# Optimization experiments

Measured on AMD Instinct MI355X. Metric: run time of the kernel, lower is better.

Reference implementation:

```python
import jax, jax.numpy as jnp
import numpy as np

D_MODEL = 2048
NUM_HEADS = 16
HEAD_DIM = D_MODEL // NUM_HEADS
D_FF = 4 * D_MODEL
B, L = 2, 2048
LN_EPS = 1e-6


def layer_norm(x, scale, bias):
    x32 = x.astype(jnp.float32)
    mu = jnp.mean(x32, axis=-1, keepdims=True)
    var = jnp.mean(jnp.square(x32 - mu), axis=-1, keepdims=True)
    return (x32 - mu) * jax.lax.rsqrt(var + LN_EPS) * scale + bias


def setup_inputs() -> dict:
    key = jax.random.key(0)
    ks = jax.random.split(key, 10)
    s = 1.0 / np.sqrt(D_MODEL)
    x = jax.random.normal(ks[0], (B, L, D_MODEL), dtype=jnp.float32)
    mask = jnp.tril(jnp.ones((L, L), dtype=bool))[None, None, :, :]  # causal [1,1,L,L]
    wq = jax.random.normal(ks[1], (D_MODEL, D_MODEL), jnp.float32) * s
    wk = jax.random.normal(ks[2], (D_MODEL, D_MODEL), jnp.float32) * s
    wv = jax.random.normal(ks[3], (D_MODEL, D_MODEL), jnp.float32) * s
    wo = jax.random.normal(ks[4], (D_MODEL, D_MODEL), jnp.float32) * s
    w1 = jax.random.normal(ks[5], (D_MODEL, D_FF), jnp.float32) * s
    b1 = jnp.zeros((D_FF,), jnp.float32)
    w2 = jax.random.normal(ks[6], (D_FF, D_MODEL), jnp.float32) * (1.0 / np.sqrt(D_FF))
    b2 = jnp.zeros((D_MODEL,), jnp.float32)
    ln1_scale = jnp.ones((D_MODEL,), jnp.float32)
    ln1_bias = jnp.zeros((D_MODEL,), jnp.float32)
    ln2_scale = jnp.ones((D_MODEL,), jnp.float32)
    ln2_bias = jnp.zeros((D_MODEL,), jnp.float32)
    return {"x": x, "mask": mask, "ln1_scale": ln1_scale, "ln1_bias": ln1_bias,
            "wq": wq, "wk": wk, "wv": wv, "wo": wo,
            "ln2_scale": ln2_scale, "ln2_bias": ln2_bias,
            "w1": w1, "b1": b1, "w2": w2, "b2": b2}


def reference(x, mask, ln1_scale, ln1_bias, wq, wk, wv, wo,
              ln2_scale, ln2_bias, w1, b1, w2, b2):
    residual = x
    h = layer_norm(x, ln1_scale, ln1_bias)
    b, l, _ = h.shape
    q = (h @ wq).reshape(b, l, NUM_HEADS, HEAD_DIM)
    k = (h @ wk).reshape(b, l, NUM_HEADS, HEAD_DIM)
    v = (h @ wv).reshape(b, l, NUM_HEADS, HEAD_DIM)
    scores = jnp.einsum('bqhd,bkhd->bhqk', q, k) / jnp.sqrt(jnp.float32(HEAD_DIM))
    scores = jnp.where(mask, scores, -100000.0)
    attn = jax.nn.softmax(scores, axis=-1)
    attn_out = jnp.einsum('bhqk,bkhd->bqhd', attn, v).reshape(b, l, D_MODEL)
    x = residual + attn_out @ wo
    mlp = jax.nn.gelu(layer_norm(x, ln2_scale, ln2_bias) @ w1 + b1)
    return x + mlp @ w2 + b2
```

## Files before the change

### kernel.cpp

```cpp
#include <hip/hip_runtime.h>
#include <hip/hip_bf16.h>

typedef unsigned short u16;
typedef __bf16 bf16x8 __attribute__((ext_vector_type(8)));
typedef float f32x4 __attribute__((ext_vector_type(4)));

#define D_MODEL 2048
#define D_FF    8192
#define NH      16
#define HD      128
#define BATCH   2
#define SEQ     2048
#define ROWS    (BATCH*SEQ)

__device__ __forceinline__ u16 f2bf(float f) {
  union { __hip_bfloat16 h; u16 u; } cv;
  cv.h = __float2bfloat16(f);
  return cv.u;
}

__device__ __forceinline__ void gload16(const u16* g, u16* l) {
  __builtin_amdgcn_global_load_lds((const __attribute__((address_space(1))) void*)g,
                                   (__attribute__((address_space(3))) void*)l,
                                   16, 0, 0);
}

__device__ __forceinline__ float gelu_f(float x) {
  const float k0 = 0.7978845608028654f, k1 = 0.044715f;
  return 0.5f * x * (1.0f + tanhf(k0 * (x + k1 * x * x * x)));
}

__global__ __launch_bounds__(256) void ln_bf16_kernel(
    const float* __restrict__ x, const float* __restrict__ sc,
    const float* __restrict__ bs, u16* __restrict__ out)
{
  __shared__ float red[8];
  const int row = blockIdx.x, t = threadIdx.x;
  const int w = t >> 6, l = t & 63;
  const float* xr = x + (size_t)row * D_MODEL;
  float4 a = ((const float4*)xr)[t*2];
  float4 b = ((const float4*)xr)[t*2+1];
  float s  = a.x+a.y+a.z+a.w + b.x+b.y+b.z+b.w;
  float s2 = a.x*a.x+a.y*a.y+a.z*a.z+a.w*a.w + b.x*b.x+b.y*b.y+b.z*b.z+b.w*b.w;
  for (int off = 32; off; off >>= 1) { s += __shfl_down(s, off); s2 += __shfl_down(s2, off); }
  if (l == 0) { red[w] = s; red[4+w] = s2; }
  __syncthreads();
  s  = red[0]+red[1]+red[2]+red[3];
  s2 = red[4]+red[5]+red[6]+red[7];
  const float mu  = s * (1.0f / D_MODEL);
  const float var = s2 * (1.0f / D_MODEL) - mu * mu;
  const float inv = rsqrtf(var + 1e-6f);
  float4 g0 = ((const float4*)sc)[t*2], g1 = ((const float4*)sc)[t*2+1];
  float4 q0 = ((const float4*)bs)[t*2], q1 = ((const float4*)bs)[t*2+1];
  union { u16 u[8]; uint4 v; } o;
  o.u[0] = f2bf((a.x-mu)*inv*g0.x + q0.x);
  o.u[1] = f2bf((a.y-mu)*inv*g0.y + q0.y);
  o.u[2] = f2bf((a.z-mu)*inv*g0.z + q0.z);
  o.u[3] = f2bf((a.w-mu)*inv*g0.w + q0.w);
  o.u[4] = f2bf((b.x-mu)*inv*g1.x + q1.x);
  o.u[5] = f2bf((b.y-mu)*inv*g1.y + q1.y);
  o.u[6] = f2bf((b.z-mu)*inv*g1.z + q1.z);
  o.u[7] = f2bf((b.w-mu)*inv*g1.w + q1.w);
  *(uint4*)(&out[(size_t)row * D_MODEL + t*8]) = o.v;
}

__global__ __launch_bounds__(256) void transpose_w(
    const float* __restrict__ in, u16* __restrict__ out, int R, int C)
{
  __shared__ float tile[64][65];
  const int t = threadIdx.x;
  const int c0 = blockIdx.x*64, r0 = blockIdx.y*64;
  const int cq = (t & 15) * 4, rb = t >> 4;
#pragma unroll
  for (int i = 0; i < 4; ++i) {
    const float4 v = *(const float4*)&in[(size_t)(r0 + rb + i*16)*C + c0 + cq];
    tile[rb + i*16][cq+0] = v.x; tile[rb + i*16][cq+1] = v.y;
    tile[rb + i*16][cq+2] = v.z; tile[rb + i*16][cq+3] = v.w;
  }
  __syncthreads();
#pragma unroll
  for (int i = 0; i < 4; ++i) {
    const int oc = rb + i*16;
    ushort4 o;
    o.x = f2bf(tile[cq+0][oc]); o.y = f2bf(tile[cq+1][oc]);
    o.z = f2bf(tile[cq+2][oc]); o.w = f2bf(tile[cq+3][oc]);
    *(ushort4*)&out[(size_t)(c0 + oc)*R + r0 + cq] = o;
  }
}

__global__ __launch_bounds__(256) void transpose_w4(
    const float* __restrict__ s0, const float* __restrict__ s1,
    const float* __restrict__ s2, const float* __restrict__ s3,
    u16* __restrict__ d0, u16* __restrict__ d1,
    u16* __restrict__ d2, u16* __restrict__ d3)
{
  __shared__ float tile[64][65];
  const int z = blockIdx.z;
  const float* in = (z == 0) ? s0 : (z == 1) ? s1 : (z == 2) ? s2 : s3;
  u16* out       = (z == 0) ? d0 : (z == 1) ? d1 : (z == 2) ? d2 : d3;
  const int t = threadIdx.x;
  const int c0 = blockIdx.x*64, r0 = blockIdx.y*64;
  const int cq = (t & 15) * 4, rb = t >> 4;
#pragma unroll
  for (int i = 0; i < 4; ++i) {
    const float4 v = *(const float4*)&in[(size_t)(r0 + rb + i*16)*D_MODEL + c0 + cq];
    tile[rb + i*16][cq+0] = v.x; tile[rb + i*16][cq+1] = v.y;
    tile[rb + i*16][cq+2] = v.z; tile[rb + i*16][cq+3] = v.w;
  }
  __syncthreads();
#pragma unroll
  for (int i = 0; i < 4; ++i) {
    const int oc = rb + i*16;
    ushort4 o;
    o.x = f2bf(tile[cq+0][oc]); o.y = f2bf(tile[cq+1][oc]);
    o.z = f2bf(tile[cq+2][oc]); o.w = f2bf(tile[cq+3][oc]);
    *(ushort4*)&out[(size_t)(c0 + oc)*D_MODEL + r0 + cq] = o;
  }
}

__global__ __launch_bounds__(256) void transpose_v(
    const u16* __restrict__ qkv, u16* __restrict__ vt)
{
  __shared__ u16 tile[32][34];
  const int t = threadIdx.x;
  const int b = blockIdx.z;
  const int c0 = blockIdx.x*32, r0 = blockIdx.y*32;
  const int col = t & 31, rb = t >> 5;
  const u16* inb = qkv + (size_t)b*SEQ*3*D_MODEL + 2*D_MODEL;
#pragma unroll
  for (int i = 0; i < 4; ++i)
    tile[rb+i*8][col] = inb[(size_t)(r0+rb+i*8)*(3*D_MODEL) + c0+col];
  __syncthreads();
  u16* ob = vt + (size_t)b*SEQ*D_MODEL;
#pragma unroll
  for (int i = 0; i < 4; ++i)
    ob[(size_t)(c0+rb+i*8)*SEQ + r0+col] = tile[col][rb+i*8];
}

template<int EPI, int BNP>
__global__ __launch_bounds__(512, 1) void gemm8p(
    const u16* __restrict__ A, const u16* __restrict__ BT,
    void* __restrict__ Cout, const float* __restrict__ bias,
    const float* __restrict__ res, int N, int K, int gridN)
{
  constexpr int GB    = BNP / 128;
  constexpr int NI    = BNP / 64;
  constexpr int BHALF = BNP * 32;
  constexpr int BUFU  = 16384 + BNP * 64;
  __shared__ __align__(16) u16 lds[2 * BUFU];
  const int t = threadIdx.x;
  const int nwg = gridDim.x;
  const int wg = (int)blockIdx.x;
  const int wgid = (wg & 7) * (nwg >> 3) + (wg >> 3);
  const int bx = wgid % gridN, by = wgid / gridN;
  const int m0 = by * 256, n0 = bx * BNP;
  const int w = t >> 6, l = t & 63;
  const int wm = w >> 2, wn = w & 3;
  const int l15 = l & 15, lq = l >> 4;

  const int srow = t >> 2;
  const int c0s  = (t & 3) ^ ((srow >> 1) & 3);
  const u16* aS0 = A  + (size_t)(m0 + srow) * K + c0s * 8;
  const u16* aS1 = A  + (size_t)(m0 + 128 + srow) * K + c0s * 8;
  const u16* bS0 = BT + (size_t)(n0 + srow) * K + c0s * 8;
  const u16* bS1 = BT + (size_t)(n0 + (GB == 2 ? 128 : 0) + srow) * K + c0s * 8;

  int offA_[2][4], offB_[NI];
#pragma unroll
  for (int mq = 0; mq < 2; ++mq)
#pragma unroll
    for (int i2 = 0; i2 < 4; ++i2) {
      const int ra = wm * 128 + mq * 64 + i2 * 16 + l15;
      offA_[mq][i2] = ra * 32 + ((lq ^ ((ra >> 1) & 3)) * 8);
    }
#pragma unroll
  for (int j = 0; j < NI; ++j) {
    const int rb = wn * (BNP / 4) + j * 16 + l15;
    offB_[j] = rb * 32 + ((lq ^ ((rb >> 1) & 3)) * 8);
  }

  f32x4 acc[8][NI] = {};
  bf16x8 bfv[NI];
  const int nt = K >> 6;

#define STAGE_A(dst, Tn, kh) { \
    gload16(aS0 + (size_t)(Tn)*64 + (kh)*32, (dst) + (kh)*8192 + t*8); \
    gload16(aS1 + (size_t)(Tn)*64 + (kh)*32, (dst) + (kh)*8192 + 4096 + t*8); }
#define STAGE_B(dst, Tn, kh) { \
    gload16(bS0 + (size_t)(Tn)*64 + (kh)*32, (dst) + 16384 + (kh)*BHALF + t*8); \
    if (GB == 2) gload16(bS1 + (size_t)(Tn)*64 + (kh)*32, (dst) + 16384 + (kh)*BHALF + 4096 + t*8); }
#define VMS { if (GB == 2) { asm volatile("s_waitcnt vmcnt(4)" ::: "memory"); } \
              else        { asm volatile("s_waitcnt vmcnt(3)" ::: "memory"); } \
              __builtin_amdgcn_sched_barrier(0); }
#define VM0 { asm volatile("s_waitcnt vmcnt(0)" ::: "memory"); __builtin_amdgcn_sched_barrier(0); }
#define NOP { }

#define PHASE(bufc, MQ, KH, DOB, STAGECODE, WAITCODE) { \
    bf16x8 af_[4]; \
    _Pragma("unroll") \
    for (int i2 = 0; i2 < 4; ++i2) \
      af_[i2] = *(const bf16x8*)&(bufc)[offA_[MQ][i2] + (KH)*8192]; \
    if (DOB) { \
      _Pragma("unroll") \
      for (int j = 0; j < NI; ++j) \
        bfv[j] = *(const bf16x8*)&(bufc)[offB_[j] + 16384 + (KH)*BHALF]; \
    } \
    STAGECODE; \
    __builtin_amdgcn_s_barrier(); \
    asm volatile("s_waitcnt lgkmcnt(0)" ::: "memory"); \
    __builtin_amdgcn_sched_barrier(0); \
    __builtin_amdgcn_s_setprio(1); \
    _Pragma("unroll") \
    for (int i2 = 0; i2 < 4; ++i2) \
      _Pragma("unroll") \
      for (int j = 0; j < NI; ++j) \
        acc[(MQ)*4 + i2][j] = __builtin_amdgcn_mfma_f32_16x16x32_bf16(af_[i2], bfv[j], acc[(MQ)*4 + i2][j], 0, 0, 0); \
    __builtin_amdgcn_s_setprio(0); \
    WAITCODE; \
    __builtin_amdgcn_s_barrier(); }

  {
    u16* b0p = lds;
    u16* b1p = &lds[BUFU];
    STAGE_A(b0p, 0, 0); STAGE_B(b0p, 0, 0); STAGE_A(b0p, 0, 1); STAGE_B(b0p, 0, 1);
    STAGE_A(b1p, 1, 0); STAGE_B(b1p, 1, 0);
  }
  VMS;
  __builtin_amdgcn_s_barrier();

  for (int T = 0; T < nt - 2; ++T) {
    u16* bufc = &lds[(T & 1) * BUFU];
    u16* bufn = &lds[((T + 1) & 1) * BUFU];
    PHASE(bufc, 0, 0, 1, STAGE_A(bufn, T + 1, 1), NOP);
    PHASE(bufc, 1, 0, 0, STAGE_B(bufn, T + 1, 1), VMS);
    PHASE(bufc, 0, 1, 1, STAGE_A(bufc, T + 2, 0), NOP);
    PHASE(bufc, 1, 1, 0, STAGE_B(bufc, T + 2, 0), NOP);
  }
  {
    u16* bufc = &lds[((nt - 2) & 1) * BUFU];
    u16* bufn = &lds[((nt - 1) & 1) * BUFU];
    PHASE(bufc, 0, 0, 1, STAGE_A(bufn, nt - 1, 1), NOP);
    PHASE(bufc, 1, 0, 0, STAGE_B(bufn, nt - 1, 1), VMS);
    PHASE(bufc, 0, 1, 1, NOP, NOP);
    PHASE(bufc, 1, 1, 0, NOP, VM0);
  }
  {
    u16* bufc = &lds[((nt - 1) & 1) * BUFU];
    PHASE(bufc, 0, 0, 1, NOP, NOP);
    PHASE(bufc, 1, 0, 0, NOP, NOP);
    PHASE(bufc, 0, 1, 1, NOP, NOP);
    PHASE(bufc, 1, 1, 0, NOP, NOP);
  }
#undef PHASE
#undef STAGE_A
#undef STAGE_B
#undef VMS
#undef VM0
#undef NOP

  const int rowb = m0 + wm * 128;
  const int colb = n0 + wn * (BNP / 4);
#pragma unroll
  for (int mi = 0; mi < 8; ++mi) {
#pragma unroll
    for (int ni = 0; ni < NI; ++ni) {
      const int col = colb + ni * 16 + l15;
      const int row0 = rowb + mi * 16 + lq * 4;
      float bv = (EPI == 2 || EPI == 3) ? bias[col] : 0.f;
#pragma unroll
      for (int r = 0; r < 4; ++r) {
        const float v = acc[mi][ni][r];
        const size_t idx = (size_t)(row0 + r) * N + col;
        if (EPI == 0)      ((u16*)Cout)[idx] = f2bf(v);
        else if (EPI == 1) ((float*)Cout)[idx] = v + res[idx];
        else if (EPI == 2) ((u16*)Cout)[idx] = f2bf(gelu_f(v + bv));
        else               ((float*)Cout)[idx] = v + bv + res[idx];
      }
    }
  }
}

__global__ __launch_bounds__(256) void attn_kernel(
    const u16* __restrict__ qkv, const u16* __restrict__ vt,
    u16* __restrict__ out)
{
  __shared__ u16 Ks[64*128];
  __shared__ u16 Vs[128*64];
  __shared__ u16 Ps[4*16*64];
  const int t = threadIdx.x;
  const int pairi = blockIdx.x & 15, bh = blockIdx.x >> 4;
  const int b = bh >> 4, h = bh & 15;
  const int w = t >> 6, l = t & 63;
  const int l15 = l & 15, lq = l >> 4;
  const size_t kbase = (size_t)b*SEQ*(3*D_MODEL) + D_MODEL + h*HD;
  const size_t vbase = (size_t)(b*SEQ + h*HD) * SEQ;
  u16* pw = &Ps[w*1024];

  for (int qsel = 0; qsel < 2; ++qsel) {
    const int qt = qsel ? (31 - pairi) : pairi;

    bf16x8 qf[4];
    {
      const u16* qb = qkv + (size_t)(b*SEQ + qt*64 + w*16 + l15)*(3*D_MODEL) + h*HD;
#pragma unroll
      for (int kk = 0; kk < 4; ++kk)
        qf[kk] = *(const bf16x8*)(qb + kk*32 + lq*8);
    }
    float m[4]    = {-INFINITY, -INFINITY, -INFINITY, -INFINITY};
    float lsum[4] = {0.f, 0.f, 0.f, 0.f};
    f32x4 acc_o[8] = {};

    for (int j = 0; j <= qt; ++j) {
      __syncthreads();
#pragma unroll
      for (int i = 0; i < 4; ++i) {
        const int o16 = i*256 + t;
        {
          const int row = o16 >> 4, cs = o16 & 15;
          const int srcc = cs ^ (row & 7);
          gload16(qkv + kbase + (size_t)(j*64+row)*(3*D_MODEL) + srcc*8, &Ks[o16*8]);
        }
        {
          const int row = o16 >> 3, cs = o16 & 7;
          const int srcc = cs ^ (row & 7);
          gload16(vt + vbase + (size_t)row*SEQ + j*64 + srcc*8, &Vs[o16*8]);
        }
      }
      __syncthreads();

      f32x4 sacc[4] = {};
#pragma unroll
      for (int nf = 0; nf < 4; ++nf) {
        const int kr = nf*16 + l15;
        const int sw = kr & 7;
#pragma unroll
        for (int kk = 0; kk < 4; ++kk) {
          bf16x8 kf = *(const bf16x8*)&Ks[kr*128 + ((kk*4+lq) ^ sw)*8];
          sacc[nf] = __builtin_amdgcn_mfma_f32_16x16x32_bf16(qf[kk], kf, sacc[nf], 0, 0, 0);
        }
      }

      const float scale = 0.08838834764831845f;
      if (j == qt) {
#pragma unroll
        for (int nf = 0; nf < 4; ++nf)
#pragma unroll
          for (int r = 0; r < 4; ++r) {
            float s = sacc[nf][r] * scale;
            const int ki = nf*16 + l15;
            const int qi = w*16 + lq*4 + r;
            if (ki > qi) s = -100000.0f;
            sacc[nf][r] = s;
          }
      } else {
#pragma unroll
        for (int nf = 0; nf < 4; ++nf)
#pragma unroll
          for (int r = 0; r < 4; ++r) sacc[nf][r] *= scale;
      }

      float scal[4];
#pragma unroll
      for (int r = 0; r < 4; ++r) {
        float mx = fmaxf(fmaxf(sacc[0][r], sacc[1][r]), fmaxf(sacc[2][r], sacc[3][r]));
#pragma unroll
        for (int off = 1; off < 16; off <<= 1)
          mx = fmaxf(mx, __shfl_xor(mx, off));
        const float mn = fmaxf(m[r], mx);
        scal[r] = __expf(m[r] - mn);
        m[r] = mn;
        float rs = 0.f;
#pragma unroll
        for (int nf = 0; nf < 4; ++nf) {
          const float p = __expf(sacc[nf][r] - mn);
          sacc[nf][r] = p;
          rs += p;
        }
#pragma unroll
        for (int off = 1; off < 16; off <<= 1)
          rs += __shfl_xor(rs, off);
        lsum[r] = lsum[r]*scal[r] + rs;
      }
#pragma unroll
      for (int nf2 = 0; nf2 < 8; ++nf2)
#pragma unroll
        for (int r = 0; r < 4; ++r) acc_o[nf2][r] *= scal[r];

#pragma unroll
      for (int nf = 0; nf < 4; ++nf)
#pragma unroll
        for (int r = 0; r < 4; ++r) {
          const int qr = lq*4 + r, kc = nf*16 + l15;
          pw[qr*64 + (((kc>>3) ^ (qr&7))*8 + (kc&7))] = f2bf(sacc[nf][r]);
        }

#pragma unroll
      for (int kk2 = 0; kk2 < 2; ++kk2) {
        bf16x8 pf = *(const bf16x8*)&pw[l15*64 + (((kk2*4+lq) ^ (l15&7))*8)];
#pragma unroll
        for (int nf2 = 0; nf2 < 8; ++nf2) {
          const int vr = nf2*16 + l15;
          bf16x8 vf = *(const bf16x8*)&Vs[vr*64 + ((kk2*4+lq) ^ (vr&7))*8];
          acc_o[nf2] = __builtin_amdgcn_mfma_f32_16x16x32_bf16(pf, vf, acc_o[nf2], 0, 0, 0);
        }
      }
    }

    const size_t ro = (size_t)(b*SEQ + qt*64 + w*16 + lq*4);
#pragma unroll
    for (int r = 0; r < 4; ++r) {
      const float inv = 1.0f / lsum[r];
#pragma unroll
      for (int nf2 = 0; nf2 < 8; ++nf2)
        out[(ro + r)*D_MODEL + h*HD + nf2*16 + l15] = f2bf(acc_o[nf2][r] * inv);
    }
    __syncthreads();
  }
}

extern "C" void kernel_launch(void* const* d_in, const int* in_sizes, int n_in,
                              void* d_out, int out_size, void* d_ws, size_t ws_size,
                              hipStream_t stream)
{
  (void)in_sizes; (void)n_in; (void)out_size; (void)ws_size;
  const float* x    = (const float*)d_in[0];
  const float* ln1s = (const float*)d_in[2];
  const float* ln1b = (const float*)d_in[3];
  const float* wq   = (const float*)d_in[4];
  const float* wk   = (const float*)d_in[5];
  const float* wv   = (const float*)d_in[6];
  const float* wo   = (const float*)d_in[7];
  const float* ln2s = (const float*)d_in[8];
  const float* ln2b = (const float*)d_in[9];
  const float* w1   = (const float*)d_in[10];
  const float* b1   = (const float*)d_in[11];
  const float* w2   = (const float*)d_in[12];
  const float* b2   = (const float*)d_in[13];
  float* out = (float*)d_out;

  char* ws = (char*)d_ws;
  constexpr size_t OFF_WQKV = 0;
  constexpr size_t OFF_WO   = OFF_WQKV + (size_t)3*D_MODEL*D_MODEL*2;
  constexpr size_t OFF_W1   = OFF_WO   + (size_t)D_MODEL*D_MODEL*2;
  constexpr size_t OFF_W2   = OFF_W1   + (size_t)D_FF*D_MODEL*2;
  constexpr size_t OFF_H    = OFF_W2   + (size_t)D_MODEL*D_FF*2;
  constexpr size_t OFF_QKV  = OFF_H    + (size_t)ROWS*D_MODEL*2;
  constexpr size_t OFF_VT   = OFF_QKV  + (size_t)ROWS*3*D_MODEL*2;
  constexpr size_t OFF_ATTN = OFF_VT   + (size_t)ROWS*D_MODEL*2;
  constexpr size_t OFF_X2   = OFF_ATTN + (size_t)ROWS*D_MODEL*2;

  u16*   wqkv_bt = (u16*)(ws + OFF_WQKV);
  u16*   wo_bt   = (u16*)(ws + OFF_WO);
  u16*   w1_bt   = (u16*)(ws + OFF_W1);
  u16*   w2_bt   = (u16*)(ws + OFF_W2);
  u16*   h_bf    = (u16*)(ws + OFF_H);
  u16*   qkv     = (u16*)(ws + OFF_QKV);
  u16*   vt      = (u16*)(ws + OFF_VT);
  u16*   act     = qkv;
  u16*   attn    = (u16*)(ws + OFF_ATTN);
  float* x2      = (float*)(ws + OFF_X2);

  const dim3 B256(256), B512(512);

  transpose_w4<<<dim3(32,32,4), B256, 0, stream>>>(
      wq, wk, wv, wo,
      wqkv_bt, wqkv_bt + (size_t)D_MODEL*D_MODEL, wqkv_bt + (size_t)2*D_MODEL*D_MODEL, wo_bt);
  transpose_w<<<dim3(128,32), B256, 0, stream>>>(w1, w1_bt, D_MODEL, D_FF);
  transpose_w<<<dim3(32,128), B256, 0, stream>>>(w2, w2_bt, D_FF, D_MODEL);

  ln_bf16_kernel<<<ROWS, B256, 0, stream>>>(x, ln1s, ln1b, h_bf);
  gemm8p<0,128><<<dim3(768), B512, 0, stream>>>(h_bf, wqkv_bt, qkv, nullptr, nullptr, 3*D_MODEL, D_MODEL, 48);
  transpose_v<<<dim3(64,64,2), B256, 0, stream>>>(qkv, vt);
  attn_kernel<<<dim3(BATCH*NH*16), B256, 0, stream>>>(qkv, vt, attn);
  gemm8p<1,128><<<dim3(256), B512, 0, stream>>>(attn, wo_bt, (void*)x2, nullptr, x, D_MODEL, D_MODEL, 16);
  ln_bf16_kernel<<<ROWS, B256, 0, stream>>>(x2, ln2s, ln2b, h_bf);
  gemm8p<2,256><<<dim3(512), B512, 0, stream>>>(h_bf, w1_bt, act, b1, nullptr, D_FF, D_MODEL, 32);
  gemm8p<3,128><<<dim3(256), B512, 0, stream>>>(act, w2_bt, (void*)out, b2, x2, D_MODEL, D_FF, 16);
}
```

Before: 649.8 us.

## Share 128-key K/V tiles between paired query tiles in attention kernel

```diff
diff --git a/kernel.cpp b/kernel.cpp
--- a/kernel.cpp
+++ b/kernel.cpp
@@ -284,9 +284,9 @@
     const u16* __restrict__ qkv, const u16* __restrict__ vt,
     u16* __restrict__ out)
 {
-  __shared__ u16 Ks[64*128];
-  __shared__ u16 Vs[128*64];
-  __shared__ u16 Ps[4*16*64];
+  __shared__ u16 Ks[128*128];
+  __shared__ u16 Vs[128*128];
+  __shared__ u16 Ps[4*16*128];
   const int t = threadIdx.x;
   const int pairi = blockIdx.x & 15, bh = blockIdx.x >> 4;
   const int b = bh >> 4, h = bh & 15;
@@ -294,127 +294,144 @@
   const int l15 = l & 15, lq = l >> 4;
   const size_t kbase = (size_t)b*SEQ*(3*D_MODEL) + D_MODEL + h*HD;
   const size_t vbase = (size_t)(b*SEQ + h*HD) * SEQ;
-  u16* pw = &Ps[w*1024];
-
-  for (int qsel = 0; qsel < 2; ++qsel) {
-    const int qt = qsel ? (31 - pairi) : pairi;
-
-    bf16x8 qf[4];
-    {
-      const u16* qb = qkv + (size_t)(b*SEQ + qt*64 + w*16 + l15)*(3*D_MODEL) + h*HD;
-#pragma unroll
-      for (int kk = 0; kk < 4; ++kk)
-        qf[kk] = *(const bf16x8*)(qb + kk*32 + lq*8);
-    }
-    float m[4]    = {-INFINITY, -INFINITY, -INFINITY, -INFINITY};
-    float lsum[4] = {0.f, 0.f, 0.f, 0.f};
-    f32x4 acc_o[8] = {};
-
-    for (int j = 0; j <= qt; ++j) {
-      __syncthreads();
-#pragma unroll
-      for (int i = 0; i < 4; ++i) {
-        const int o16 = i*256 + t;
-        {
-          const int row = o16 >> 4, cs = o16 & 15;
-          const int srcc = cs ^ (row & 7);
-          gload16(qkv + kbase + (size_t)(j*64+row)*(3*D_MODEL) + srcc*8, &Ks[o16*8]);
-        }
-        {
-          const int row = o16 >> 3, cs = o16 & 7;
-          const int srcc = cs ^ (row & 7);
-          gload16(vt + vbase + (size_t)row*SEQ + j*64 + srcc*8, &Vs[o16*8]);
-        }
-      }
-      __syncthreads();
-
-      f32x4 sacc[4] = {};
-#pragma unroll
-      for (int nf = 0; nf < 4; ++nf) {
-        const int kr = nf*16 + l15;
-        const int sw = kr & 7;
-#pragma unroll
-        for (int kk = 0; kk < 4; ++kk) {
-          bf16x8 kf = *(const bf16x8*)&Ks[kr*128 + ((kk*4+lq) ^ sw)*8];
-          sacc[nf] = __builtin_amdgcn_mfma_f32_16x16x32_bf16(qf[kk], kf, sacc[nf], 0, 0, 0);
-        }
-      }
-
-      const float scale = 0.08838834764831845f;
-      if (j == qt) {
-#pragma unroll
-        for (int nf = 0; nf < 4; ++nf)
-#pragma unroll
-          for (int r = 0; r < 4; ++r) {
-            float s = sacc[nf][r] * scale;
-            const int ki = nf*16 + l15;
-            const int qi = w*16 + lq*4 + r;
-            if (ki > qi) s = -100000.0f;
-            sacc[nf][r] = s;
-          }
-      } else {
-#pragma unroll
-        for (int nf = 0; nf < 4; ++nf)
-#pragma unroll
-          for (int r = 0; r < 4; ++r) sacc[nf][r] *= scale;
-      }
-
-      float scal[4];
-#pragma unroll
-      for (int r = 0; r < 4; ++r) {
-        float mx = fmaxf(fmaxf(sacc[0][r], sacc[1][r]), fmaxf(sacc[2][r], sacc[3][r]));
-#pragma unroll
-        for (int off = 1; off < 16; off <<= 1)
-          mx = fmaxf(mx, __shfl_xor(mx, off));
-        const float mn = fmaxf(m[r], mx);
-        scal[r] = __expf(m[r] - mn);
-        m[r] = mn;
-        float rs = 0.f;
-#pragma unroll
-        for (int nf = 0; nf < 4; ++nf) {
-          const float p = __expf(sacc[nf][r] - mn);
-          sacc[nf][r] = p;
-          rs += p;
-        }
-#pragma unroll
-        for (int off = 1; off < 16; off <<= 1)
-          rs += __shfl_xor(rs, off);
-        lsum[r] = lsum[r]*scal[r] + rs;
-      }
+  u16* pw = &Ps[w*2048];
+
+  const int qtS = pairi, qtL = 31 - pairi;
+  const int jmaxS = qtS >> 1, jmaxL = qtL >> 1;
+  const float scale = 0.08838834764831845f;
+
+  bf16x8 qfS[4], qfL[4];
+  {
+    const u16* qbS = qkv + (size_t)(b*SEQ + qtS*64 + w*16 + l15)*(3*D_MODEL) + h*HD;
+    const u16* qbL = qkv + (size_t)(b*SEQ + qtL*64 + w*16 + l15)*(3*D_MODEL) + h*HD;
+#pragma unroll
+    for (int kk = 0; kk < 4; ++kk) {
+      qfS[kk] = *(const bf16x8*)(qbS + kk*32 + lq*8);
+      qfL[kk] = *(const bf16x8*)(qbL + kk*32 + lq*8);
+    }
+  }
+  float mS[4], mL[4], lsS[4], lsL[4];
+#pragma unroll
+  for (int r = 0; r < 4; ++r) { mS[r] = -INFINITY; mL[r] = -INFINITY; lsS[r] = 0.f; lsL[r] = 0.f; }
+  f32x4 accS[8] = {}, accL[8] = {};
+
+#define COMPUTE(QT, JMAX, QF, MM, LS, ACC) { \
+    f32x4 sacc[8]; \
+    _Pragma("unroll") \
+    for (int nf = 0; nf < 8; ++nf) sacc[nf] = (f32x4){0.f,0.f,0.f,0.f}; \
+    _Pragma("unroll") \
+    for (int nf = 0; nf < 8; ++nf) { \
+      const int kr = nf*16 + l15; \
+      const int sw = kr & 7; \
+      _Pragma("unroll") \
+      for (int kk = 0; kk < 4; ++kk) { \
+        bf16x8 kf = *(const bf16x8*)&Ks[kr*128 + ((kk*4+lq) ^ sw)*8]; \
+        sacc[nf] = __builtin_amdgcn_mfma_f32_16x16x32_bf16(QF[kk], kf, sacc[nf], 0, 0, 0); \
+      } \
+    } \
+    if (j == (JMAX)) { \
+      _Pragma("unroll") \
+      for (int nf = 0; nf < 8; ++nf) \
+        _Pragma("unroll") \
+        for (int r = 0; r < 4; ++r) { \
+          float s = sacc[nf][r] * scale; \
+          const int ki = j*128 + nf*16 + l15; \
+          const int qi = (QT)*64 + w*16 + lq*4 + r; \
+          if (ki > qi) s = -100000.0f; \
+          sacc[nf][r] = s; \
+        } \
+    } else { \
+      _Pragma("unroll") \
+      for (int nf = 0; nf < 8; ++nf) \
+        _Pragma("unroll") \
+        for (int r = 0; r < 4; ++r) sacc[nf][r] *= scale; \
+    } \
+    float scal[4]; \
+    _Pragma("unroll") \
+    for (int r = 0; r < 4; ++r) { \
+      float mx = sacc[0][r]; \
+      _Pragma("unroll") \
+      for (int nf = 1; nf < 8; ++nf) mx = fmaxf(mx, sacc[nf][r]); \
+      _Pragma("unroll") \
+      for (int off = 1; off < 16; off <<= 1) mx = fmaxf(mx, __shfl_xor(mx, off)); \
+      const float mn = fmaxf(MM[r], mx); \
+      scal[r] = __expf(MM[r] - mn); \
+      MM[r] = mn; \
+      float rs = 0.f; \
+      _Pragma("unroll") \
+      for (int nf = 0; nf < 8; ++nf) { \
+        const float p = __expf(sacc[nf][r] - mn); \
+        sacc[nf][r] = p; \
+        rs += p; \
+      } \
+      _Pragma("unroll") \
+      for (int off = 1; off < 16; off <<= 1) rs += __shfl_xor(rs, off); \
+      LS[r] = LS[r]*scal[r] + rs; \
+    } \
+    _Pragma("unroll") \
+    for (int nf2 = 0; nf2 < 8; ++nf2) \
+      _Pragma("unroll") \
+      for (int r = 0; r < 4; ++r) ACC[nf2][r] *= scal[r]; \
+    _Pragma("unroll") \
+    for (int nf = 0; nf < 8; ++nf) \
+      _Pragma("unroll") \
+      for (int r = 0; r < 4; ++r) { \
+        const int qr = lq*4 + r, kc = nf*16 + l15; \
+        pw[qr*128 + (((kc>>3) ^ (qr&7))*8 + (kc&7))] = f2bf(sacc[nf][r]); \
+      } \
+    _Pragma("unroll") \
+    for (int kk2 = 0; kk2 < 4; ++kk2) { \
+      bf16x8 pf = *(const bf16x8*)&pw[l15*128 + (((kk2*4+lq) ^ (l15&7))*8)]; \
+      _Pragma("unroll") \
+      for (int nf2 = 0; nf2 < 8; ++nf2) { \
+        const int vr = nf2*16 + l15; \
+        bf16x8 vf = *(const bf16x8*)&Vs[vr*128 + ((kk2*4+lq) ^ (vr&7))*8]; \
+        ACC[nf2] = __builtin_amdgcn_mfma_f32_16x16x32_bf16(pf, vf, ACC[nf2], 0, 0, 0); \
+      } \
+    } }
+
+  for (int j = 0; j <= jmaxL; ++j) {
+    __syncthreads();
+#pragma unroll
+    for (int i = 0; i < 8; ++i) {
+      const int o16 = i*256 + t;
+      const int row = o16 >> 4, cs = o16 & 15;
+      const int srcc = cs ^ (row & 7);
+      gload16(qkv + kbase + (size_t)(j*128+row)*(3*D_MODEL) + srcc*8, &Ks[o16*8]);
+    }
+#pragma unroll
+    for (int i = 0; i < 8; ++i) {
+      const int o16 = i*256 + t;
+      const int row = o16 >> 4, cs = o16 & 15;
+      const int srcc = cs ^ (row & 7);
+      gload16(vt + vbase + (size_t)row*SEQ + j*128 + srcc*8, &Vs[o16*8]);
+    }
+    __syncthreads();
+
+    COMPUTE(qtL, jmaxL, qfL, mL, lsL, accL);
+    if (j <= jmaxS) COMPUTE(qtS, jmaxS, qfS, mS, lsS, accS);
+  }
+#undef COMPUTE
+
+  {
+    const size_t ro = (size_t)(b*SEQ + qtL*64 + w*16 + lq*4);
+#pragma unroll
+    for (int r = 0; r < 4; ++r) {
+      const float inv = 1.0f / lsL[r];
 #pragma unroll
       for (int nf2 = 0; nf2 < 8; ++nf2)
-#pragma unroll
-        for (int r = 0; r < 4; ++r) acc_o[nf2][r] *= scal[r];
-
-#pragma unroll
-      for (int nf = 0; nf < 4; ++nf)
-#pragma unroll
-        for (int r = 0; r < 4; ++r) {
-          const int qr = lq*4 + r, kc = nf*16 + l15;
-          pw[qr*64 + (((kc>>3) ^ (qr&7))*8 + (kc&7))] = f2bf(sacc[nf][r]);
-        }
-
-#pragma unroll
-      for (int kk2 = 0; kk2 < 2; ++kk2) {
-        bf16x8 pf = *(const bf16x8*)&pw[l15*64 + (((kk2*4+lq) ^ (l15&7))*8)];
-#pragma unroll
-        for (int nf2 = 0; nf2 < 8; ++nf2) {
-          const int vr = nf2*16 + l15;
-          bf16x8 vf = *(const bf16x8*)&Vs[vr*64 + ((kk2*4+lq) ^ (vr&7))*8];
-          acc_o[nf2] = __builtin_amdgcn_mfma_f32_16x16x32_bf16(pf, vf, acc_o[nf2], 0, 0, 0);
-        }
-      }
-    }
-
-    const size_t ro = (size_t)(b*SEQ + qt*64 + w*16 + lq*4);
+        out[(ro + r)*D_MODEL + h*HD + nf2*16 + l15] = f2bf(accL[nf2][r] * inv);
+    }
+  }
+  {
+    const size_t ro = (size_t)(b*SEQ + qtS*64 + w*16 + lq*4);
 #pragma unroll
     for (int r = 0; r < 4; ++r) {
-      const float inv = 1.0f / lsum[r];
+      const float inv = 1.0f / lsS[r];
 #pragma unroll
       for (int nf2 = 0; nf2 < 8; ++nf2)
-        out[(ro + r)*D_MODEL + h*HD + nf2*16 + l15] = f2bf(acc_o[nf2][r] * inv);
-    }
-    __syncthreads();
+        out[(ro + r)*D_MODEL + h*HD + nf2*16 + l15] = f2bf(accS[nf2][r] * inv);
+    }
   }
 }
 
```

Result: slower. 680.6 us (+4.7%).
